# Optimization experiments

Hardware: AMD Instinct MI355X
Metric: run time of the kernel (lower is better)

Reference implementation:

```python
import jax, jax.numpy as jnp
import numpy as np

NUM_HEADS = 8
HEAD_DIM = 64  # d_model 512 / 8 heads


def rope(x):
    # x: (B, S, D). Rotary applied over the FULL hidden dim (as in source),
    # with even/odd halves CONCATENATED (not interleaved) on output.
    b, s, d = x.shape
    pos = jnp.arange(s, dtype=jnp.float32)[:, None]                      # (S, 1)
    freqs = jnp.exp(jnp.arange(0, d, 2, dtype=jnp.float32) * (-np.log(10000.0) / d))  # (D/2,)
    ang = pos * freqs                                                     # (S, D/2)
    cos = jnp.cos(ang)[None, :, :]
    sin = jnp.sin(ang)[None, :, :]
    xe = x[..., 0::2]
    xo = x[..., 1::2]
    return jnp.concatenate([xe * cos - xo * sin, xo * cos + xe * sin], axis=-1)


def split_heads(x):
    b, s, d = x.shape
    return x.reshape(b, s, NUM_HEADS, HEAD_DIM).transpose(0, 2, 1, 3)  # (B,H,S,hd)


def setup_inputs() -> dict:
    key = jax.random.key(0)
    ks = jax.random.split(key, 8)
    B, S, D = 2, 2048, 512
    sc = 1.0 / np.sqrt(D)
    return {
        "querys": jax.random.normal(ks[0], (B, S, D), jnp.float32),
        "keys": jax.random.normal(ks[1], (B, S, D), jnp.float32),
        "values": jax.random.normal(ks[2], (B, S, D), jnp.float32),
        "attn_mask": jnp.zeros((B, 1, S, S), jnp.float32),
        "Wq": jax.random.normal(ks[3], (D, D), jnp.float32) * sc,
        "Wk": jax.random.normal(ks[4], (D, D), jnp.float32) * sc,
        "Wv": jax.random.normal(ks[5], (D, D), jnp.float32) * sc,
        "Wo": jax.random.normal(ks[6], (D, D), jnp.float32) * sc,
    }


def reference(querys, keys, values, attn_mask, Wq, Wk, Wv, Wo):
    q = split_heads(rope(querys @ Wq.T))   # (B,H,Sq,hd)
    k = split_heads(rope(keys @ Wk.T))     # (B,H,Sk,hd)
    v = split_heads(values @ Wv.T)         # (B,H,Sk,hd)

    logits = jnp.einsum("bhqd,bhkd->bhqk", q, k)
    # mask added BEFORE scaling, exactly as in the source
    logits = logits + attn_mask[:, :, : q.shape[2], : k.shape[2]] * (-1e9)
    attn_scores = jax.nn.softmax(logits / np.float32(HEAD_DIM) ** 0.5, axis=-1)

    embeds = jnp.einsum("bhqk,bhkd->bhqd", attn_scores, v)
    b, h, s, hd = embeds.shape
    embeds = embeds.transpose(0, 2, 1, 3).reshape(b, s, h * hd) @ Wo.T
    return embeds, attn_scores
```

## Files before the change

### kernel.cpp

```cpp
#include <hip/hip_runtime.h>
#include <hip/hip_fp16.h>

typedef _Float16 f16x8 __attribute__((ext_vector_type(8)));
typedef float f32x16 __attribute__((ext_vector_type(16)));

#define LOG2E 1.44269504088896340736f

typedef __attribute__((address_space(1))) const unsigned char gl_byte;
typedef __attribute__((address_space(3))) unsigned char lds_byte;

#define GLOAD_LDS16(g, l) \
  __builtin_amdgcn_global_load_lds((const gl_byte*)(g), (lds_byte*)(l), 16, 0, 0)

static __device__ __forceinline__ f32x16 zero16() {
  f32x16 z;
#pragma unroll
  for (int i = 0; i < 16; ++i) z[i] = 0.0f;
  return z;
}

static __device__ __forceinline__ unsigned pkh(float a, float b) {
  union { _Float16 h[2]; unsigned u; } t;
  t.h[0] = (_Float16)a; t.h[1] = (_Float16)b;
  return t.u;
}

static __device__ __forceinline__ void swap32(unsigned x, unsigned y, int hi,
                                              unsigned& a, unsigned& c) {
  unsigned py = (unsigned)__shfl_xor((int)y, 32);
  unsigned px = (unsigned)__shfl_xor((int)x, 32);
  a = hi ? py : x;
  c = hi ? y : px;
}

static __device__ __forceinline__ void stage_k64(char* dst,
                                                 const _Float16* __restrict__ kr,
                                                 int b, int h, int kb, int tid) {
#pragma unroll
  for (int it = 0; it < 4; ++it) {
    int s = it * 128 + tid;
    int r = s >> 3, c8 = (s & 7) ^ (r & 7);
    const _Float16* g = kr + (size_t)(b * 2048 + kb * 64 + r) * 512 + h * 64 + c8 * 8;
    GLOAD_LDS16(g, dst + (it * 128 + (tid & 64)) * 16);
  }
}

__global__ __launch_bounds__(256) void proj_kernel(
    const float* __restrict__ qin, const float* __restrict__ kin,
    const float* __restrict__ vin, const float* __restrict__ Wq,
    const float* __restrict__ Wk, const float* __restrict__ Wv,
    _Float16* __restrict__ q_r, _Float16* __restrict__ k_r,
    _Float16* __restrict__ v_t) {
  __shared__ char smem[8192 + 16384];
  const int tid = threadIdx.x;
  const int l = tid & 63, lo = l & 31, hi = l >> 5;
  const int w = tid >> 6, wm = w >> 1, wn = w & 1;
  const int m0 = blockIdx.y * 64, n0 = blockIdx.x * 128;
  const int zz = blockIdx.z;
  const float* A = zz == 0 ? qin : zz == 1 ? kin : vin;
  const float* W = zz == 0 ? Wq : zz == 1 ? Wk : Wv;

  f32x16 acc[2];
  acc[0] = zero16();
  acc[1] = zero16();

  for (int kb = 0; kb < 8; ++kb) {
#pragma unroll
    for (int i = 0; i < 4; ++i) {
      int idx = tid + 256 * i; int r = idx >> 4, c4 = idx & 15;
      float4 v = *(const float4*)(A + (size_t)(m0 + r) * 512 + kb * 64 + c4 * 4);
      uint2 uu; uu.x = pkh(v.x, v.y); uu.y = pkh(v.z, v.w);
      *(uint2*)(smem + ((r * 128 + c4 * 8) ^ ((r & 7) << 4))) = uu;
    }
#pragma unroll
    for (int i = 0; i < 8; ++i) {
      int idx = tid + 256 * i; int r = idx >> 4, c4 = idx & 15;
      float4 v = *(const float4*)(W + (size_t)(n0 + r) * 512 + kb * 64 + c4 * 4);
      uint2 uu; uu.x = pkh(v.x, v.y); uu.y = pkh(v.z, v.w);
      *(uint2*)(smem + 8192 + ((r * 128 + c4 * 8) ^ ((r & 7) << 4))) = uu;
    }
    __syncthreads();
#pragma unroll
    for (int ks = 0; ks < 4; ++ks) {
      int ra = wm * 32 + lo;
      f16x8 a0 = *(const f16x8*)(smem + ((ra * 128 + ks * 32 + hi * 16) ^ ((ra & 7) << 4)));
      int rb0 = wn * 64 + lo, rb1 = rb0 + 32;
      f16x8 b0 = *(const f16x8*)(smem + 8192 + ((rb0 * 128 + ks * 32 + hi * 16) ^ ((rb0 & 7) << 4)));
      f16x8 b1 = *(const f16x8*)(smem + 8192 + ((rb1 * 128 + ks * 32 + hi * 16) ^ ((rb1 & 7) << 4)));
      acc[0] = __builtin_amdgcn_mfma_f32_32x32x16_f16(a0, b0, acc[0], 0, 0, 0);
      acc[1] = __builtin_amdgcn_mfma_f32_32x32x16_f16(a0, b1, acc[1], 0, 0, 0);
    }
    __syncthreads();
  }

  if (zz < 2) {
    _Float16* out = zz ? k_r : q_r;
#pragma unroll
    for (int nt = 0; nt < 2; ++nt) {
      int n = n0 + wn * 64 + nt * 32 + lo;
      int odd = lo & 1;
      int ii = (n >> 1) & 255;
      float fr = exp2f(-(float)ii * 0.05190512648261504f);
#pragma unroll
      for (int r = 0; r < 16; ++r) {
        int m = m0 + wm * 32 + (r & 3) + 8 * ((r >> 2) & 3) + 4 * hi;
        float a = acc[nt][r];
        float bb = __shfl_xor(a, 1);
        float xe = odd ? bb : a, xo = odd ? a : bb;
        float ang = (float)(m & 2047) * fr;
        float sn, cs;
        sincosf(ang, &sn, &cs);
        float res = odd ? (xo * cs + xe * sn) : (xe * cs - xo * sn);
        out[(size_t)m * 512 + ii + (odd ? 256 : 0)] = (_Float16)res;
      }
    }
  } else {
#pragma unroll
    for (int nt = 0; nt < 2; ++nt) {
      int n = n0 + wn * 64 + nt * 32 + lo;
      int hh = n >> 6, d = n & 63;
#pragma unroll
      for (int a = 0; a < 4; ++a) {
        int m = m0 + wm * 32 + 8 * a + 4 * hi;
        int b_ = m >> 11, s = m & 2047;
        uint2 uu;
        uu.x = pkh(acc[nt][4 * a + 0], acc[nt][4 * a + 1]);
        uu.y = pkh(acc[nt][4 * a + 2], acc[nt][4 * a + 3]);
        *(uint2*)(v_t + (size_t)((b_ * 8 + hh) * 64 + d) * 2048 + s) = uu;
      }
    }
  }
}

__global__ __launch_bounds__(256) void out_gemm(const float* __restrict__ opart,
                                                const float* __restrict__ W,
                                                float* __restrict__ out) {
  __shared__ char smem[8192 + 16384];
  const int tid = threadIdx.x;
  const int l = tid & 63, lo = l & 31, hi = l >> 5;
  const int w = tid >> 6, wm = w >> 1, wn = w & 1;
  const int m0 = blockIdx.y * 64, n0 = blockIdx.x * 128;

  f32x16 acc[2];
  acc[0] = zero16();
  acc[1] = zero16();

  for (int kb = 0; kb < 8; ++kb) {
#pragma unroll
    for (int i = 0; i < 4; ++i) {
      int idx = tid + 256 * i; int r = idx >> 4, c4 = idx & 15;
      size_t off = (size_t)(m0 + r) * 512 + kb * 64 + c4 * 4;
      float4 x = *(const float4*)(opart + off);
      float4 y = *(const float4*)(opart + (size_t)4096 * 512 + off);
      float4 u = *(const float4*)(opart + (size_t)2 * 4096 * 512 + off);
      float4 t = *(const float4*)(opart + (size_t)3 * 4096 * 512 + off);
      uint2 uu;
      uu.x = pkh(x.x + y.x + u.x + t.x, x.y + y.y + u.y + t.y);
      uu.y = pkh(x.z + y.z + u.z + t.z, x.w + y.w + u.w + t.w);
      *(uint2*)(smem + ((r * 128 + c4 * 8) ^ ((r & 7) << 4))) = uu;
    }
#pragma unroll
    for (int i = 0; i < 8; ++i) {
      int idx = tid + 256 * i; int r = idx >> 4, c4 = idx & 15;
      float4 v = *(const float4*)(W + (size_t)(n0 + r) * 512 + kb * 64 + c4 * 4);
      uint2 uu; uu.x = pkh(v.x, v.y); uu.y = pkh(v.z, v.w);
      *(uint2*)(smem + 8192 + ((r * 128 + c4 * 8) ^ ((r & 7) << 4))) = uu;
    }
    __syncthreads();
#pragma unroll
    for (int ks = 0; ks < 4; ++ks) {
      int ra = wm * 32 + lo;
      f16x8 a0 = *(const f16x8*)(smem + ((ra * 128 + ks * 32 + hi * 16) ^ ((ra & 7) << 4)));
      int rb0 = wn * 64 + lo, rb1 = rb0 + 32;
      f16x8 b0 = *(const f16x8*)(smem + 8192 + ((rb0 * 128 + ks * 32 + hi * 16) ^ ((rb0 & 7) << 4)));
      f16x8 b1 = *(const f16x8*)(smem + 8192 + ((rb1 * 128 + ks * 32 + hi * 16) ^ ((rb1 & 7) << 4)));
      acc[0] = __builtin_amdgcn_mfma_f32_32x32x16_f16(a0, b0, acc[0], 0, 0, 0);
      acc[1] = __builtin_amdgcn_mfma_f32_32x32x16_f16(a0, b1, acc[1], 0, 0, 0);
    }
    __syncthreads();
  }

  {
#pragma unroll
    for (int nt = 0; nt < 2; ++nt) {
      int n = n0 + wn * 64 + nt * 32 + lo;
#pragma unroll
      for (int r = 0; r < 16; ++r) {
        int m = m0 + wm * 32 + (r & 3) + 8 * ((r >> 2) & 3) + 4 * hi;
        out[(size_t)m * 512 + n] = acc[nt][r];
      }
    }
  }
}

__global__ __launch_bounds__(256) void mask_scan(const float* __restrict__ mask,
                                                 int* __restrict__ flag) {
  const int n4 = 2 * 2048 * 2048 / 4;
  bool nz = false;
  for (int i = blockIdx.x * 256 + threadIdx.x; i < n4; i += gridDim.x * 256) {
    float4 v = ((const float4*)mask)[i];
    nz |= (v.x != 0.f) || (v.y != 0.f) || (v.z != 0.f) || (v.w != 0.f);
  }
  if (__any(nz) && (threadIdx.x & 63) == 0) atomicOr(flag, 1);
}

__global__ __launch_bounds__(128, 4) void lsum_kernel(
    const _Float16* __restrict__ qr, const _Float16* __restrict__ kr,
    const float* __restrict__ mask, const int* __restrict__ flagp,
    float* __restrict__ lsums) {
  __shared__ char smem[16384];
  const int tid = threadIdx.x;
  const int w = tid >> 6, l = tid & 63, lo = l & 31, hi = l >> 5;
  const int bh = blockIdx.y, b = bh >> 3, h = bh & 7;
  const int q0 = blockIdx.x * 64, z = blockIdx.z;
  const int mflag = *flagp;
  const float C = 0.125f * LOG2E;
  const int qw = q0 + w * 32 + lo;

  f16x8 qf[4];
  {
    const _Float16* qrow = qr + (size_t)(b * 2048 + qw) * 512 + h * 64 + hi * 8;
#pragma unroll
    for (int ks = 0; ks < 4; ++ks) qf[ks] = *(const f16x8*)(qrow + ks * 16);
  }

  const int kb0 = z * 8;
  stage_k64(smem, kr, b, h, kb0, tid);
  __syncthreads();

  float lsum = 0.f;
  for (int t = 0; t < 8; ++t) {
    const int cur = t & 1, kb = kb0 + t;
    if (t < 7) stage_k64(smem + (cur ^ 1) * 8192, kr, b, h, kb + 1, tid);
    char* kbuf = smem + cur * 8192;
#pragma unroll
    for (int ks4 = 0; ks4 < 2; ++ks4) {
      f32x16 acc = zero16();
      int krw = ks4 * 32 + lo;
#pragma unroll
      for (int ks = 0; ks < 4; ++ks) {
        f16x8 kf = *(const f16x8*)(kbuf + ((krw * 128 + ks * 32 + hi * 16) ^ ((krw & 7) << 4)));
        acc = __builtin_amdgcn_mfma_f32_32x32x16_f16(kf, qf[ks], acc, 0, 0, 0);
      }
      if (!mflag) {
#pragma unroll
        for (int r = 0; r < 16; ++r) lsum += exp2f(acc[r] * C);
      } else {
#pragma unroll
        for (int r = 0; r < 16; ++r) {
          int kg = kb * 64 + ks4 * 32 + (r & 3) + 8 * ((r >> 2) & 3) + 4 * hi;
          float mv = mask[(size_t)(b * 2048 + qw) * 2048 + kg];
          lsum += exp2f((acc[r] - 1e9f * mv) * C);
        }
      }
    }
    __syncthreads();
  }
  lsum += __shfl_xor(lsum, 32);
  if (hi == 0) lsums[(size_t)(z * 16 + bh) * 2048 + qw] = lsum;
}

__global__ __launch_bounds__(128, 3) void attn_kernel(
    const _Float16* __restrict__ qr, const _Float16* __restrict__ kr,
    const _Float16* __restrict__ vt, const float* __restrict__ mask,
    const int* __restrict__ flagp, const float* __restrict__ lsums,
    float* __restrict__ scores, float* __restrict__ opart) {
  __shared__ char smem[24576];
  const int tid = threadIdx.x;
  const int w = tid >> 6, l = tid & 63, lo = l & 31, hi = l >> 5;
  const int bh = blockIdx.y, b = bh >> 3, h = bh & 7;
  const int q0 = blockIdx.x * 64, z = blockIdx.z;
  const int mflag = *flagp;
  const float C = 0.125f * LOG2E;
  const int qw = q0 + w * 32 + lo;

  f16x8 qf[4];
  {
    const _Float16* qrow = qr + (size_t)(b * 2048 + qw) * 512 + h * 64 + hi * 8;
#pragma unroll
    for (int ks = 0; ks < 4; ++ks) qf[ks] = *(const f16x8*)(qrow + ks * 16);
  }

  float lsum = 0.f;
#pragma unroll
  for (int zz = 0; zz < 4; ++zz) lsum += lsums[(size_t)(zz * 16 + bh) * 2048 + qw];
  const float inv = 1.0f / lsum;

  f32x16 oacc[2];
  oacc[0] = zero16();
  oacc[1] = zero16();
  char* trw = smem + 16384 + (w << 12);
  const _Float16* vbase = vt + (size_t)((b * 8 + h) * 64) * 2048;

  const int kb0 = z * 8;
  stage_k64(smem, kr, b, h, kb0, tid);
  __syncthreads();

  for (int t = 0; t < 8; ++t) {
    const int cur = t & 1, kb = kb0 + t;
    if (t < 7) stage_k64(smem + (cur ^ 1) * 8192, kr, b, h, kb + 1, tid);
    f16x8 vp[8];
#pragma unroll
    for (int f = 0; f < 8; ++f) {
      int ks4 = f >> 2, kb2 = (f >> 1) & 1, dt = f & 1;
      int d = dt * 32 + lo;
      vp[f] = *(const f16x8*)(vbase + (size_t)d * 2048 + kb * 64 + ks4 * 32 + kb2 * 16 + hi * 8);
    }
    char* kbuf = smem + cur * 8192;
#pragma unroll
    for (int ks4 = 0; ks4 < 2; ++ks4) {
      f32x16 acc = zero16();
      int krw = ks4 * 32 + lo;
#pragma unroll
      for (int ks = 0; ks < 4; ++ks) {
        f16x8 kf = *(const f16x8*)(kbuf + ((krw * 128 + ks * 32 + hi * 16) ^ ((krw & 7) << 4)));
        acc = __builtin_amdgcn_mfma_f32_32x32x16_f16(kf, qf[ks], acc, 0, 0, 0);
      }
      float p[16];
      if (!mflag) {
#pragma unroll
        for (int r = 0; r < 16; ++r) p[r] = exp2f(acc[r] * C) * inv;
      } else {
#pragma unroll
        for (int r = 0; r < 16; ++r) {
          int kg = kb * 64 + ks4 * 32 + (r & 3) + 8 * ((r >> 2) & 3) + 4 * hi;
          float mv = mask[(size_t)(b * 2048 + qw) * 2048 + kg];
          p[r] = exp2f((acc[r] - 1e9f * mv) * C) * inv;
        }
      }
#pragma unroll
      for (int r = 0; r < 16; ++r) {
        int krow = (r & 3) + 8 * ((r >> 2) & 3) + 4 * hi;
        *(float*)(trw + lo * 128 + (((krow ^ lo) & 31) << 2)) = p[r];
      }
      float* srow = scores + (size_t)(bh * 2048 + q0 + w * 32) * 2048 + kb * 64 + ks4 * 32;
      {
        int qrd = l >> 3, m4 = (l & 7) << 2;
#pragma unroll
        for (int j = 0; j < 4; ++j) {
          int q = qrd + 8 * j;
          int g = (m4 ^ (q & 28)) & 31;
          float4 v = *(const float4*)(trw + q * 128 + g * 4);
          const float* vf = (const float*)&v;
          int px = q & 3;
          float4 o;
          o.x = vf[0 ^ px]; o.y = vf[1 ^ px]; o.z = vf[2 ^ px]; o.w = vf[3 ^ px];
          *(float4*)(srow + (size_t)q * 2048 + m4) = o;
        }
      }
#pragma unroll
      for (int kb2 = 0; kb2 < 2; ++kb2) {
        unsigned X0 = pkh(p[8 * kb2 + 0], p[8 * kb2 + 1]);
        unsigned X1 = pkh(p[8 * kb2 + 2], p[8 * kb2 + 3]);
        unsigned Y0 = pkh(p[8 * kb2 + 4], p[8 * kb2 + 5]);
        unsigned Y1 = pkh(p[8 * kb2 + 6], p[8 * kb2 + 7]);
        unsigned w0, w1, w2, w3;
        swap32(X0, Y0, hi, w0, w2);
        swap32(X1, Y1, hi, w1, w3);
        union { unsigned u[4]; f16x8 v; } pf;
        pf.u[0] = w0; pf.u[1] = w1; pf.u[2] = w2; pf.u[3] = w3;
#pragma unroll
        for (int dt = 0; dt < 2; ++dt)
          oacc[dt] = __builtin_amdgcn_mfma_f32_32x32x16_f16(vp[ks4 * 4 + kb2 * 2 + dt],
                                                            pf.v, oacc[dt], 0, 0, 0);
      }
    }
    __syncthreads();
  }
  float* orow = opart + (size_t)z * 4096 * 512 + (size_t)(b * 2048 + qw) * 512 + h * 64;
#pragma unroll
  for (int dt = 0; dt < 2; ++dt)
#pragma unroll
    for (int a = 0; a < 4; ++a) {
      int d = dt * 32 + 8 * a + 4 * hi;
      float4 o;
      o.x = oacc[dt][4 * a + 0]; o.y = oacc[dt][4 * a + 1];
      o.z = oacc[dt][4 * a + 2]; o.w = oacc[dt][4 * a + 3];
      *(float4*)(orow + d) = o;
    }
}

extern "C" void kernel_launch(void* const* d_in, const int* in_sizes, int n_in,
                              void* d_out, int out_size, void* d_ws, size_t ws_size,
                              hipStream_t stream) {
  const float* querys = (const float*)d_in[0];
  const float* keys   = (const float*)d_in[1];
  const float* values = (const float*)d_in[2];
  const float* mask   = (const float*)d_in[3];
  const float* Wq = (const float*)d_in[4];
  const float* Wk = (const float*)d_in[5];
  const float* Wv = (const float*)d_in[6];
  const float* Wo = (const float*)d_in[7];

  char* ws = (char*)d_ws;
  const size_t MB = 1048576;
  _Float16* q_r  = (_Float16*)(ws + 0 * MB);
  _Float16* k_r  = (_Float16*)(ws + 4 * MB);
  _Float16* v_t  = (_Float16*)(ws + 8 * MB);
  float*    opart = (float*)(ws + 12 * MB);
  float*    lsums = (float*)(ws + 44 * MB);
  int*      flag  = (int*)(ws + 45 * MB);

  float* out_sc = (float*)d_out + (size_t)4096 * 512;

  hipMemsetAsync(flag, 0, 4, stream);
  mask_scan<<<dim3(1024), 256, 0, stream>>>(mask, flag);

  proj_kernel<<<dim3(4, 64, 3), 256, 0, stream>>>(querys, keys, values, Wq, Wk, Wv,
                                                  q_r, k_r, v_t);

  lsum_kernel<<<dim3(32, 16, 4), 128, 0, stream>>>(q_r, k_r, mask, flag, lsums);

  attn_kernel<<<dim3(32, 16, 4), 128, 0, stream>>>(q_r, k_r, v_t, mask, flag, lsums,
                                                   out_sc, opart);

  out_gemm<<<dim3(4, 64), 256, 0, stream>>>(opart, Wo, (float*)d_out);
}
```

Baseline: 209.5 us.

## Fuse mask scan into projection, store fp16 partials, widen lsum blocks, defer score stores

The mask-nonzero scan becomes an extra z-slice of the projection kernel, which drops one launch and lets the scan overlap the GEMMs. Attention partial outputs are stored as fp16 instead of fp32, halving the write and re-read traffic between attn_kernel and out_gemm at some precision cost. lsum_kernel moves to 256-thread blocks covering 128 queries with a matching K staging helper. In attn_kernel, V fragment loads are split per half-tile to cut register pressure, and score stores are buffered in registers and issued after the barrier.

```diff
diff --git a/kernel.cpp b/kernel.cpp
--- a/kernel.cpp
+++ b/kernel.cpp
@@ -2,6 +2,7 @@
 #include <hip/hip_fp16.h>
 
 typedef _Float16 f16x8 __attribute__((ext_vector_type(8)));
+typedef _Float16 f16x4 __attribute__((ext_vector_type(4)));
 typedef float f32x16 __attribute__((ext_vector_type(16)));
 
 #define LOG2E 1.44269504088896340736f
@@ -45,18 +46,46 @@
   }
 }
 
+static __device__ __forceinline__ void stage_k64_256(char* dst,
+                                                     const _Float16* __restrict__ kr,
+                                                     int b, int h, int kb, int tid) {
+#pragma unroll
+  for (int it = 0; it < 2; ++it) {
+    int s = it * 256 + tid;
+    int r = s >> 3, c8 = (s & 7) ^ (r & 7);
+    const _Float16* g = kr + (size_t)(b * 2048 + kb * 64 + r) * 512 + h * 64 + c8 * 8;
+    GLOAD_LDS16(g, dst + (it * 256 + (tid & 192)) * 16);
+  }
+}
+
 __global__ __launch_bounds__(256) void proj_kernel(
     const float* __restrict__ qin, const float* __restrict__ kin,
     const float* __restrict__ vin, const float* __restrict__ Wq,
     const float* __restrict__ Wk, const float* __restrict__ Wv,
+    const float* __restrict__ mask, int* __restrict__ flag,
     _Float16* __restrict__ q_r, _Float16* __restrict__ k_r,
     _Float16* __restrict__ v_t) {
   __shared__ char smem[8192 + 16384];
   const int tid = threadIdx.x;
+  const int zz = blockIdx.z;
+
+  if (zz == 3) {
+    int bid = blockIdx.y * 4 + blockIdx.x;
+    const float4* m4p = (const float4*)mask;
+    int base = bid * 8192 + tid;
+    bool nz = false;
+#pragma unroll 4
+    for (int i = 0; i < 32; ++i) {
+      float4 v = m4p[base + i * 256];
+      nz |= (v.x != 0.f) || (v.y != 0.f) || (v.z != 0.f) || (v.w != 0.f);
+    }
+    if (__any(nz) && (tid & 63) == 0) atomicOr(flag, 1);
+    return;
+  }
+
   const int l = tid & 63, lo = l & 31, hi = l >> 5;
   const int w = tid >> 6, wm = w >> 1, wn = w & 1;
   const int m0 = blockIdx.y * 64, n0 = blockIdx.x * 128;
-  const int zz = blockIdx.z;
   const float* A = zz == 0 ? qin : zz == 1 ? kin : vin;
   const float* W = zz == 0 ? Wq : zz == 1 ? Wk : Wv;
 
@@ -132,7 +161,7 @@
   }
 }
 
-__global__ __launch_bounds__(256) void out_gemm(const float* __restrict__ opart,
+__global__ __launch_bounds__(256) void out_gemm(const _Float16* __restrict__ opart,
                                                 const float* __restrict__ W,
                                                 float* __restrict__ out) {
   __shared__ char smem[8192 + 16384];
@@ -140,6 +169,7 @@
   const int l = tid & 63, lo = l & 31, hi = l >> 5;
   const int w = tid >> 6, wm = w >> 1, wn = w & 1;
   const int m0 = blockIdx.y * 64, n0 = blockIdx.x * 128;
+  const size_t slab = (size_t)4096 * 512;
 
   f32x16 acc[2];
   acc[0] = zero16();
@@ -150,13 +180,15 @@
     for (int i = 0; i < 4; ++i) {
       int idx = tid + 256 * i; int r = idx >> 4, c4 = idx & 15;
       size_t off = (size_t)(m0 + r) * 512 + kb * 64 + c4 * 4;
-      float4 x = *(const float4*)(opart + off);
-      float4 y = *(const float4*)(opart + (size_t)4096 * 512 + off);
-      float4 u = *(const float4*)(opart + (size_t)2 * 4096 * 512 + off);
-      float4 t = *(const float4*)(opart + (size_t)3 * 4096 * 512 + off);
-      uint2 uu;
-      uu.x = pkh(x.x + y.x + u.x + t.x, x.y + y.y + u.y + t.y);
-      uu.y = pkh(x.z + y.z + u.z + t.z, x.w + y.w + u.w + t.w);
+      f16x4 x = *(const f16x4*)(opart + off);
+      f16x4 y = *(const f16x4*)(opart + slab + off);
+      f16x4 u = *(const f16x4*)(opart + 2 * slab + off);
+      f16x4 t = *(const f16x4*)(opart + 3 * slab + off);
+      float s0 = (float)x[0] + (float)y[0] + (float)u[0] + (float)t[0];
+      float s1 = (float)x[1] + (float)y[1] + (float)u[1] + (float)t[1];
+      float s2 = (float)x[2] + (float)y[2] + (float)u[2] + (float)t[2];
+      float s3 = (float)x[3] + (float)y[3] + (float)u[3] + (float)t[3];
+      uint2 uu; uu.x = pkh(s0, s1); uu.y = pkh(s2, s3);
       *(uint2*)(smem + ((r * 128 + c4 * 8) ^ ((r & 7) << 4))) = uu;
     }
 #pragma unroll
@@ -180,31 +212,18 @@
     __syncthreads();
   }
 
-  {
-#pragma unroll
-    for (int nt = 0; nt < 2; ++nt) {
-      int n = n0 + wn * 64 + nt * 32 + lo;
-#pragma unroll
-      for (int r = 0; r < 16; ++r) {
-        int m = m0 + wm * 32 + (r & 3) + 8 * ((r >> 2) & 3) + 4 * hi;
-        out[(size_t)m * 512 + n] = acc[nt][r];
-      }
-    }
-  }
-}
-
-__global__ __launch_bounds__(256) void mask_scan(const float* __restrict__ mask,
-                                                 int* __restrict__ flag) {
-  const int n4 = 2 * 2048 * 2048 / 4;
-  bool nz = false;
-  for (int i = blockIdx.x * 256 + threadIdx.x; i < n4; i += gridDim.x * 256) {
-    float4 v = ((const float4*)mask)[i];
-    nz |= (v.x != 0.f) || (v.y != 0.f) || (v.z != 0.f) || (v.w != 0.f);
-  }
-  if (__any(nz) && (threadIdx.x & 63) == 0) atomicOr(flag, 1);
-}
-
-__global__ __launch_bounds__(128, 4) void lsum_kernel(
+#pragma unroll
+  for (int nt = 0; nt < 2; ++nt) {
+    int n = n0 + wn * 64 + nt * 32 + lo;
+#pragma unroll
+    for (int r = 0; r < 16; ++r) {
+      int m = m0 + wm * 32 + (r & 3) + 8 * ((r >> 2) & 3) + 4 * hi;
+      out[(size_t)m * 512 + n] = acc[nt][r];
+    }
+  }
+}
+
+__global__ __launch_bounds__(256, 4) void lsum_kernel(
     const _Float16* __restrict__ qr, const _Float16* __restrict__ kr,
     const float* __restrict__ mask, const int* __restrict__ flagp,
     float* __restrict__ lsums) {
@@ -212,7 +231,7 @@
   const int tid = threadIdx.x;
   const int w = tid >> 6, l = tid & 63, lo = l & 31, hi = l >> 5;
   const int bh = blockIdx.y, b = bh >> 3, h = bh & 7;
-  const int q0 = blockIdx.x * 64, z = blockIdx.z;
+  const int q0 = blockIdx.x * 128, z = blockIdx.z;
   const int mflag = *flagp;
   const float C = 0.125f * LOG2E;
   const int qw = q0 + w * 32 + lo;
@@ -225,13 +244,13 @@
   }
 
   const int kb0 = z * 8;
-  stage_k64(smem, kr, b, h, kb0, tid);
+  stage_k64_256(smem, kr, b, h, kb0, tid);
   __syncthreads();
 
   float lsum = 0.f;
   for (int t = 0; t < 8; ++t) {
     const int cur = t & 1, kb = kb0 + t;
-    if (t < 7) stage_k64(smem + (cur ^ 1) * 8192, kr, b, h, kb + 1, tid);
+    if (t < 7) stage_k64_256(smem + (cur ^ 1) * 8192, kr, b, h, kb + 1, tid);
     char* kbuf = smem + cur * 8192;
 #pragma unroll
     for (int ks4 = 0; ks4 < 2; ++ks4) {
@@ -264,7 +283,7 @@
     const _Float16* __restrict__ qr, const _Float16* __restrict__ kr,
     const _Float16* __restrict__ vt, const float* __restrict__ mask,
     const int* __restrict__ flagp, const float* __restrict__ lsums,
-    float* __restrict__ scores, float* __restrict__ opart) {
+    float* __restrict__ scores, _Float16* __restrict__ opart) {
   __shared__ char smem[24576];
   const int tid = threadIdx.x;
   const int w = tid >> 6, l = tid & 63, lo = l & 31, hi = l >> 5;
@@ -291,6 +310,7 @@
   oacc[1] = zero16();
   char* trw = smem + 16384 + (w << 12);
   const _Float16* vbase = vt + (size_t)((b * 8 + h) * 64) * 2048;
+  const int qrd = l >> 3, m4 = (l & 7) << 2;
 
   const int kb0 = z * 8;
   stage_k64(smem, kr, b, h, kb0, tid);
@@ -299,14 +319,8 @@
   for (int t = 0; t < 8; ++t) {
     const int cur = t & 1, kb = kb0 + t;
     if (t < 7) stage_k64(smem + (cur ^ 1) * 8192, kr, b, h, kb + 1, tid);
-    f16x8 vp[8];
-#pragma unroll
-    for (int f = 0; f < 8; ++f) {
-      int ks4 = f >> 2, kb2 = (f >> 1) & 1, dt = f & 1;
-      int d = dt * 32 + lo;
-      vp[f] = *(const f16x8*)(vbase + (size_t)d * 2048 + kb * 64 + ks4 * 32 + kb2 * 16 + hi * 8);
-    }
     char* kbuf = smem + cur * 8192;
+    float4 so[2][4];
 #pragma unroll
     for (int ks4 = 0; ks4 < 2; ++ks4) {
       f32x16 acc = zero16();
@@ -315,6 +329,13 @@
       for (int ks = 0; ks < 4; ++ks) {
         f16x8 kf = *(const f16x8*)(kbuf + ((krw * 128 + ks * 32 + hi * 16) ^ ((krw & 7) << 4)));
         acc = __builtin_amdgcn_mfma_f32_32x32x16_f16(kf, qf[ks], acc, 0, 0, 0);
+      }
+      f16x8 vp[4];
+#pragma unroll
+      for (int f = 0; f < 4; ++f) {
+        int kb2 = f >> 1, dt = f & 1;
+        int d = dt * 32 + lo;
+        vp[f] = *(const f16x8*)(vbase + (size_t)d * 2048 + kb * 64 + ks4 * 32 + kb2 * 16 + hi * 8);
       }
       float p[16];
       if (!mflag) {
@@ -333,20 +354,16 @@
         int krow = (r & 3) + 8 * ((r >> 2) & 3) + 4 * hi;
         *(float*)(trw + lo * 128 + (((krow ^ lo) & 31) << 2)) = p[r];
       }
-      float* srow = scores + (size_t)(bh * 2048 + q0 + w * 32) * 2048 + kb * 64 + ks4 * 32;
-      {
-        int qrd = l >> 3, m4 = (l & 7) << 2;
-#pragma unroll
-        for (int j = 0; j < 4; ++j) {
-          int q = qrd + 8 * j;
-          int g = (m4 ^ (q & 28)) & 31;
-          float4 v = *(const float4*)(trw + q * 128 + g * 4);
-          const float* vf = (const float*)&v;
-          int px = q & 3;
-          float4 o;
-          o.x = vf[0 ^ px]; o.y = vf[1 ^ px]; o.z = vf[2 ^ px]; o.w = vf[3 ^ px];
-          *(float4*)(srow + (size_t)q * 2048 + m4) = o;
-        }
+#pragma unroll
+      for (int j = 0; j < 4; ++j) {
+        int q = qrd + 8 * j;
+        int g = (m4 ^ (q & 28)) & 31;
+        float4 v = *(const float4*)(trw + q * 128 + g * 4);
+        const float* vf = (const float*)&v;
+        int px = q & 3;
+        float4 o;
+        o.x = vf[0 ^ px]; o.y = vf[1 ^ px]; o.z = vf[2 ^ px]; o.w = vf[3 ^ px];
+        so[ks4][j] = o;
       }
 #pragma unroll
       for (int kb2 = 0; kb2 < 2; ++kb2) {
@@ -361,22 +378,31 @@
         pf.u[0] = w0; pf.u[1] = w1; pf.u[2] = w2; pf.u[3] = w3;
 #pragma unroll
         for (int dt = 0; dt < 2; ++dt)
-          oacc[dt] = __builtin_amdgcn_mfma_f32_32x32x16_f16(vp[ks4 * 4 + kb2 * 2 + dt],
+          oacc[dt] = __builtin_amdgcn_mfma_f32_32x32x16_f16(vp[kb2 * 2 + dt],
                                                             pf.v, oacc[dt], 0, 0, 0);
       }
     }
     __syncthreads();
-  }
-  float* orow = opart + (size_t)z * 4096 * 512 + (size_t)(b * 2048 + qw) * 512 + h * 64;
+#pragma unroll
+    for (int ks4 = 0; ks4 < 2; ++ks4) {
+      float* srow = scores + (size_t)(bh * 2048 + q0 + w * 32) * 2048 + kb * 64 + ks4 * 32;
+#pragma unroll
+      for (int j = 0; j < 4; ++j) {
+        int q = qrd + 8 * j;
+        *(float4*)(srow + (size_t)q * 2048 + m4) = so[ks4][j];
+      }
+    }
+  }
+  _Float16* orow = opart + (size_t)z * 4096 * 512 + (size_t)(b * 2048 + qw) * 512 + h * 64;
 #pragma unroll
   for (int dt = 0; dt < 2; ++dt)
 #pragma unroll
     for (int a = 0; a < 4; ++a) {
       int d = dt * 32 + 8 * a + 4 * hi;
-      float4 o;
-      o.x = oacc[dt][4 * a + 0]; o.y = oacc[dt][4 * a + 1];
-      o.z = oacc[dt][4 * a + 2]; o.w = oacc[dt][4 * a + 3];
-      *(float4*)(orow + d) = o;
+      uint2 uu;
+      uu.x = pkh(oacc[dt][4 * a + 0], oacc[dt][4 * a + 1]);
+      uu.y = pkh(oacc[dt][4 * a + 2], oacc[dt][4 * a + 3]);
+      *(uint2*)(orow + d) = uu;
     }
 }
 
@@ -394,22 +420,21 @@
 
   char* ws = (char*)d_ws;
   const size_t MB = 1048576;
-  _Float16* q_r  = (_Float16*)(ws + 0 * MB);
-  _Float16* k_r  = (_Float16*)(ws + 4 * MB);
-  _Float16* v_t  = (_Float16*)(ws + 8 * MB);
-  float*    opart = (float*)(ws + 12 * MB);
-  float*    lsums = (float*)(ws + 44 * MB);
-  int*      flag  = (int*)(ws + 45 * MB);
+  _Float16* q_r   = (_Float16*)(ws + 0 * MB);
+  _Float16* k_r   = (_Float16*)(ws + 4 * MB);
+  _Float16* v_t   = (_Float16*)(ws + 8 * MB);
+  _Float16* opart = (_Float16*)(ws + 12 * MB);
+  float*    lsums = (float*)(ws + 28 * MB);
+  int*      flag  = (int*)(ws + 29 * MB);
 
   float* out_sc = (float*)d_out + (size_t)4096 * 512;
 
   hipMemsetAsync(flag, 0, 4, stream);
-  mask_scan<<<dim3(1024), 256, 0, stream>>>(mask, flag);
-
-  proj_kernel<<<dim3(4, 64, 3), 256, 0, stream>>>(querys, keys, values, Wq, Wk, Wv,
-                                                  q_r, k_r, v_t);
-
-  lsum_kernel<<<dim3(32, 16, 4), 128, 0, stream>>>(q_r, k_r, mask, flag, lsums);
+
+  proj_kernel<<<dim3(4, 64, 4), 256, 0, stream>>>(querys, keys, values, Wq, Wk, Wv,
+                                                  mask, flag, q_r, k_r, v_t);
+
+  lsum_kernel<<<dim3(16, 16, 4), 256, 0, stream>>>(q_r, k_r, mask, flag, lsums);
 
   attn_kernel<<<dim3(32, 16, 4), 128, 0, stream>>>(q_r, k_r, v_t, mask, flag, lsums,
                                                    out_sc, opart);
```

Result: slower. 222.4 us (+6.1%).
